# Optimization experiments

Hardware: AMD Instinct MI355X
Metric: run time of the kernel (lower is better)

The kernel has to match this reference:

```python
import jax, jax.numpy as jnp
import numpy as np

N = 32          # objects in the (single) image
P = N * (N - 1) # relation pairs
D = 256         # self.dim
M = 14          # mask_size / pooler resolution
OC = 151        # obj classes
RC = 51         # rel classes
RED = D // 4    # attention gate reduction


def setup_inputs() -> dict:
    key = jax.random.key(0)
    ks = jax.random.split(key, 32)
    # all ordered pairs i != j
    ii, jj = np.meshgrid(np.arange(N), np.arange(N), indexing='ij')
    keep = ii != jj
    rel_pair_idxs = jnp.asarray(np.stack([ii[keep], jj[keep]], 1), jnp.int32)  # [P,2]
    # valid xyxy boxes in an 800x600 image
    x1 = jax.random.uniform(ks[0], (N,)) * 600.0
    y1 = jax.random.uniform(ks[1], (N,)) * 400.0
    w = jax.random.uniform(ks[2], (N,)) * 180.0 + 20.0
    h = jax.random.uniform(ks[3], (N,)) * 180.0 + 20.0
    bboxes = jnp.stack([x1, y1, x1 + w, y1 + h], 1).astype(jnp.float32)
    roi_features = jax.random.normal(ks[4], (N, 4096), jnp.float32)
    predict_logits = jax.random.normal(ks[5], (N, OC), jnp.float32)
    union_features = jax.random.normal(ks[6], (P, D, M, M), jnp.float32)
    s = 0.02
    p = dict(
        roi_features=roi_features, bboxes=bboxes, predict_logits=predict_logits,
        union_features=union_features, rel_pair_idxs=rel_pair_idxs,
        W_emb1=jax.random.normal(ks[7], (4096 + OC + 4, D)) * s, b_emb1=jnp.zeros((D,)),
        W_emb2=jax.random.normal(ks[8], (D, D)) * s, b_emb2=jnp.zeros((D,)),
        # stacked SE-attention gates: 0=sbj, 1=obj, 2=bg
        att_fc1_w=jax.random.normal(ks[9], (3, D, RED)) * s, att_fc1_b=jnp.zeros((3, RED)),
        att_fc2_w=jax.random.normal(ks[10], (3, RED, D)) * s, att_fc2_b=jnp.zeros((3, D)),
        W_c1=jax.random.normal(ks[11], (3 * D, D)) * s, b_c1=jnp.zeros((D,)),
        W_c2=jax.random.normal(ks[12], (D, D)) * s, b_c2=jnp.zeros((D,)),
        W_gcn=jax.random.normal(ks[13], (D, D)) * s, b_gcn=jnp.zeros((D,)),
        W_objp=jax.random.normal(ks[14], (D, OC)) * s, b_objp=jnp.zeros((OC,)),
        W_relp=jax.random.normal(ks[15], (D, RC)) * s, b_relp=jnp.zeros((RC,)),
    )
    return p


def _rect_masks(x0, y0, x1, y1):
    # mask[p, r, c] = 1 iff x0<=r<x1 and y0<=c<y1  (matches torch slice write)
    r = jnp.arange(M, dtype=jnp.float32)
    rm = (r[None, :] >= x0[:, None]) & (r[None, :] < x1[:, None])  # [P,M]
    cm = (r[None, :] >= y0[:, None]) & (r[None, :] < y1[:, None])  # [P,M]
    return (rm[:, :, None] & cm[:, None, :]).astype(jnp.float32)   # [P,M,M]


def _masking(union_features, bboxes, pairs):
    sb = bboxes[pairs[:, 0]]  # [P,4]
    ob = bboxes[pairs[:, 1]]
    ux1 = jnp.minimum(sb[:, 0], ob[:, 0])
    uy1 = jnp.minimum(sb[:, 1], ob[:, 1])
    x = jnp.stack([sb[:, 0], sb[:, 2], ob[:, 0], ob[:, 2]], 1) - ux1[:, None]
    y = jnp.stack([sb[:, 1], sb[:, 3], ob[:, 1], ob[:, 3]], 1) - uy1[:, None]
    xr = M / jnp.maximum(x[:, 1], x[:, 3])
    yr = M / jnp.maximum(y[:, 1], y[:, 3])
    xp = jnp.round(x * xr[:, None])
    yp = jnp.round(y * yr[:, None])
    sm = _rect_masks(xp[:, 0], yp[:, 0], xp[:, 1], yp[:, 1])[:, None]  # [P,1,M,M]
    om = _rect_masks(xp[:, 2], yp[:, 2], xp[:, 3], yp[:, 3])[:, None]
    bm = jnp.clip(1.0 - sm - om, 0.0, 1.0)
    return union_features * sm, union_features * om, union_features * bm


def _att_gate(x, w1, b1, w2, b2):
    # SE-style channel attention gate
    s = x.mean((2, 3))                                        # [P,D]
    g = jax.nn.sigmoid(jax.nn.relu(s @ w1 + b1) @ w2 + b2)    # [P,D]
    return x * g[:, :, None, None]


def _adjacency(pairs):
    o2o = jnp.zeros((N, N)).at[pairs[:, 0], pairs[:, 1]].set(1.0)
    ar = jnp.arange(P)
    o2r = jnp.zeros((N, P)).at[pairs[:, 0], ar].set(1.0).at[pairs[:, 1], ar].set(1.0)
    top = jnp.concatenate([o2o, o2r], 1)                     # [N, N+P]
    bot = jnp.concatenate([o2r.T, jnp.zeros((P, P))], 1)     # [P, N+P]
    adj = jnp.concatenate([top, bot], 0)
    return adj + jnp.eye(N + P)


def reference(roi_features, bboxes, predict_logits, union_features, rel_pair_idxs,
              W_emb1, b_emb1, W_emb2, b_emb2,
              att_fc1_w, att_fc1_b, att_fc2_w, att_fc2_b,
              W_c1, b_c1, W_c2, b_c2, W_gcn, b_gcn,
              W_objp, b_objp, W_relp, b_relp):
    pairs = rel_pair_idxs
    # object embedding
    obj_in = jnp.concatenate([roi_features, predict_logits, bboxes], 1)  # [N,4251]
    obj_feats = jax.nn.relu(obj_in @ W_emb1 + b_emb1) @ W_emb2 + b_emb2  # [N,D]
    # masking + attention gates + global avg pool
    sbj, obj, bg = _masking(union_features, bboxes, pairs)
    sbj = _att_gate(sbj, att_fc1_w[0], att_fc1_b[0], att_fc2_w[0], att_fc2_b[0]).mean((2, 3))
    obj = _att_gate(obj, att_fc1_w[1], att_fc1_b[1], att_fc2_w[1], att_fc2_b[1]).mean((2, 3))
    bg = _att_gate(bg, att_fc1_w[2], att_fc1_b[2], att_fc2_w[2], att_fc2_b[2]).mean((2, 3))
    # relational embedding (compose)
    rel = jnp.concatenate([sbj, obj, bg], 1)                 # [P,3D]
    rel_feats = jax.nn.relu(rel @ W_c1 + b_c1) @ W_c2 + b_c2  # [P,D]
    # GCN over object+relation graph (row-normalized adjacency, residual)
    adj = _adjacency(pairs)
    feats = jnp.concatenate([obj_feats, rel_feats], 0)        # [N+P,D]
    norm_adj = adj / adj.sum(1, keepdims=True)
    gcn_out = jax.nn.relu(norm_adj @ (feats @ W_gcn) + b_gcn) + feats
    obj_dists = gcn_out[:N] @ W_objp + b_objp                 # [N,OC]
    rel_dists = gcn_out[N:] @ W_relp + b_relp                 # [P,RC]
    return obj_dists, rel_dists
```

## Files before the change

### kernel.cpp

```cpp
#include <hip/hip_runtime.h>
#include <cstdint>
#include <cstddef>

#define NOBJ 32
#define NP   992
#define DD   256
#define SP   196
#define OC   151
#define RC   51
#define RED  64
#define KIN  4251
#define CH   128
#define KPC  34

#define OFF_PART   0u
#define OFF_OBJF   1048576u
#define OFF_SALL   1056768u
#define OFF_RELF   1818624u
#define OFF_H      2072576u
#define OFF_W2T    2334720u
#define OFF_WC1T   2400256u
#define OFF_WC2T   2596864u
#define OFF_WGT    2662400u
#define OFF_FC1WT  2727936u
#define OFF_FC2WT  2777088u
#define OFF_WOPT   2826240u
#define OFF_WRPT   2864896u

#define TR_TOT 543232

__global__ void k_pre(const float* __restrict__ uf,
                      const float* __restrict__ bbox,
                      const int* __restrict__ pairs,
                      const float* __restrict__ roi,
                      const float* __restrict__ logits,
                      const float* __restrict__ W1,
                      const float* __restrict__ W2,  const float* __restrict__ Wc1,
                      const float* __restrict__ Wc2, const float* __restrict__ Wg,
                      const float* __restrict__ f1w, const float* __restrict__ f2w,
                      const float* __restrict__ Wop, const float* __restrict__ Wrp,
                      float* __restrict__ sAll, float* __restrict__ part,
                      float* __restrict__ W2T,  float* __restrict__ Wc1T,
                      float* __restrict__ Wc2T, float* __restrict__ WgT,
                      float* __restrict__ f1wT, float* __restrict__ f2wT,
                      float* __restrict__ WopT, float* __restrict__ WrpT) {
  const int b = blockIdx.x, t = threadIdx.x;
  if (b < NP) {
    const int p = b;
    __shared__ __align__(16) float tile[64 * SP + 64];
    __shared__ __align__(16) float wS[256];
    __shared__ __align__(16) float wO[256];
    __shared__ __align__(16) float wB[256];
    __shared__ float pacc[3][4][64];
    if (t < SP) {
      int si = pairs[2 * p], oi = pairs[2 * p + 1];
      float sx1 = bbox[si * 4 + 0], sy1 = bbox[si * 4 + 1];
      float sx2 = bbox[si * 4 + 2], sy2 = bbox[si * 4 + 3];
      float ox1 = bbox[oi * 4 + 0], oy1 = bbox[oi * 4 + 1];
      float ox2 = bbox[oi * 4 + 2], oy2 = bbox[oi * 4 + 3];
      float ux = fminf(sx1, ox1), uy = fminf(sy1, oy1);
      float xr = 14.f / fmaxf(sx2 - ux, ox2 - ux);
      float yr = 14.f / fmaxf(sy2 - uy, oy2 - uy);
      float xs0 = rintf((sx1 - ux) * xr), xs1 = rintf((sx2 - ux) * xr);
      float xo0 = rintf((ox1 - ux) * xr), xo1 = rintf((ox2 - ux) * xr);
      float ys0 = rintf((sy1 - uy) * yr), ys1 = rintf((sy2 - uy) * yr);
      float yo0 = rintf((oy1 - uy) * yr), yo1 = rintf((oy2 - uy) * yr);
      int a = t / 14, bb = t - a * 14;
      float fa = (float)a, fb = (float)bb;
      float sm = (fa >= xs0 && fa < xs1 && fb >= ys0 && fb < ys1) ? 1.f : 0.f;
      float om = (fa >= xo0 && fa < xo1 && fb >= yo0 && fb < yo1) ? 1.f : 0.f;
      float bm = fminf(fmaxf(1.f - sm - om, 0.f), 1.f);
      wS[t] = sm; wO[t] = om; wB[t] = bm;
    } else {
      wS[t] = 0.f; wO[t] = 0.f; wB[t] = 0.f;
    }
    if (t < 64) tile[64 * SP + t] = 0.f;
    __syncthreads();
    const int c = t >> 2, q = t & 3;
    const float* row = tile + c * SP + q * 52;
    const float* mS = wS + q * 52;
    const float* mO = wO + q * 52;
    const float* mB = wB + q * 52;
    const float inv = 1.f / 196.f;
#pragma unroll 1
    for (int ti = 0; ti < 4; ++ti) {
      const float4* src4 = (const float4*)(uf + (size_t)p * (DD * SP) + ti * (64 * SP));
      float4* dst4 = (float4*)tile;
      for (int f = t; f < 64 * SP / 4; f += 256) dst4[f] = src4[f];
      __syncthreads();
      float a0 = 0.f, a1 = 0.f, a2 = 0.f;
#pragma unroll
      for (int g = 0; g < 13; ++g) {
        float4 v  = *(const float4*)&row[4 * g];
        float4 ms = *(const float4*)&mS[4 * g];
        float4 mo = *(const float4*)&mO[4 * g];
        float4 mb = *(const float4*)&mB[4 * g];
        a0 += v.x * ms.x + v.y * ms.y + v.z * ms.z + v.w * ms.w;
        a1 += v.x * mo.x + v.y * mo.y + v.z * mo.z + v.w * mo.w;
        a2 += v.x * mb.x + v.y * mb.y + v.z * mb.z + v.w * mb.w;
      }
      pacc[0][q][c] = a0; pacc[1][q][c] = a1; pacc[2][q][c] = a2;
      __syncthreads();
      if (t < 192) {
        int m = t >> 6, c2 = t & 63;
        float s = pacc[m][0][c2] + pacc[m][1][c2] + pacc[m][2][c2] + pacc[m][3][c2];
        sAll[(size_t)p * 768 + m * 256 + ti * 64 + c2] = s * inv;
      }
      __syncthreads();
    }
  } else if (b < NP + CH) {
    const int chunk = b - NP;
    int k0 = chunk * KPC;
    int k1 = k0 + KPC; if (k1 > KIN) k1 = KIN;
    float acc[NOBJ];
#pragma unroll
    for (int i = 0; i < NOBJ; ++i) acc[i] = 0.f;
#pragma unroll 2
    for (int k = k0; k < k1; ++k) {
      float w = W1[(size_t)k * DD + t];
      const float* xp; int stride;
      if (k < 4096)            { xp = roi    + k;               stride = 4096; }
      else if (k < 4096 + OC)  { xp = logits + (k - 4096);      stride = OC;   }
      else                     { xp = bbox   + (k - 4096 - OC); stride = 4;    }
#pragma unroll
      for (int i = 0; i < NOBJ; ++i) { acc[i] += xp[0] * w; xp += stride; }
    }
    float* pout = part + (size_t)chunk * (NOBJ * DD) + t;
#pragma unroll
    for (int i = 0; i < NOBJ; ++i) pout[i * DD] = acc[i];
  } else {
    for (int o = (b - NP - CH) * 256 + t; o < TR_TOT; o += 256 * 256) {
      float v; float* dst;
      if (o < 65536)       { int q = o;          v = W2 [(q & 255) * 256 + (q >> 8)]; dst = W2T  + q; }
      else if (o < 262144) { int q = o - 65536;  int c = q / 768, k = q - c * 768;
                             v = Wc1[k * 256 + c];                                    dst = Wc1T + q; }
      else if (o < 327680) { int q = o - 262144; v = Wc2[(q & 255) * 256 + (q >> 8)]; dst = Wc2T + q; }
      else if (o < 393216) { int q = o - 327680; v = Wg [(q & 255) * 256 + (q >> 8)]; dst = WgT  + q; }
      else if (o < 442368) { int q = o - 393216;
                             v = f1w[(q >> 14) * 16384 + (q & 255) * 64 + ((q >> 8) & 63)];
                             dst = f1wT + q; }
      else if (o < 491520) { int q = o - 442368;
                             v = f2w[(q >> 14) * 16384 + (q & 63) * 256 + ((q >> 6) & 255)];
                             dst = f2wT + q; }
      else if (o < 530176) { int q = o - 491520; v = Wop[(q & 255) * OC + (q >> 8)];  dst = WopT + q; }
      else                 { int q = o - 530176; v = Wrp[(q & 255) * RC + (q >> 8)];  dst = WrpT + q; }
      *dst = v;
    }
  }
}

__global__ void __launch_bounds__(512, 1)
k_mid2(const float* __restrict__ sAll,
       const float* __restrict__ f1wT, const float* __restrict__ f1b,
       const float* __restrict__ f2wT, const float* __restrict__ f2b,
       const float* __restrict__ Wc1T, const float* __restrict__ bc1,
       const float* __restrict__ Wc2T, const float* __restrict__ bc2,
       const float* __restrict__ WgT,
       const float* __restrict__ part, const float* __restrict__ b1,
       const float* __restrict__ W2T,  const float* __restrict__ b2,
       float* __restrict__ relf, float* __restrict__ objf,
       float* __restrict__ H) {
  const int b = blockIdx.x, t = threadIdx.x;
  const int h = t >> 8, tt = t & 255;
  __shared__ __align__(16) float sg[4][768];
  __shared__ __align__(16) float ha[4][192];
  __shared__ __align__(16) float h2[4][256];
  __shared__ __align__(16) float red[2][4][256];
  if (b < NP / 4) {
    const int p0 = b * 4;
    {
      const float4* src = (const float4*)(sAll + (size_t)p0 * 768);
      float4* dst = (float4*)&sg[0][0];
      for (int j = t; j < 768; j += 512) dst[j] = src[j];
    }
    __syncthreads();
    if (tt < 192) {
      const float4* w4 = (const float4*)(f1wT + tt * 256 + h * 128);
      const int sb = (tt >> 6) * 256 + h * 128;
      float a0 = 0, a1 = 0, a2 = 0, a3 = 0;
#pragma unroll 8
      for (int j = 0; j < 32; ++j) {
        float4 wv = w4[j];
        float4 s0 = *(const float4*)&sg[0][sb + 4 * j];
        float4 s1 = *(const float4*)&sg[1][sb + 4 * j];
        float4 s2 = *(const float4*)&sg[2][sb + 4 * j];
        float4 s3 = *(const float4*)&sg[3][sb + 4 * j];
        a0 += s0.x * wv.x + s0.y * wv.y + s0.z * wv.z + s0.w * wv.w;
        a1 += s1.x * wv.x + s1.y * wv.y + s1.z * wv.z + s1.w * wv.w;
        a2 += s2.x * wv.x + s2.y * wv.y + s2.z * wv.z + s2.w * wv.w;
        a3 += s3.x * wv.x + s3.y * wv.y + s3.z * wv.z + s3.w * wv.w;
      }
      red[h][0][tt] = a0; red[h][1][tt] = a1; red[h][2][tt] = a2; red[h][3][tt] = a3;
    }
    __syncthreads();
    if (h == 0 && tt < 192) {
      float bb = f1b[tt];
#pragma unroll
      for (int p = 0; p < 4; ++p)
        ha[p][tt] = fmaxf(red[0][p][tt] + red[1][p][tt] + bb, 0.f);
    }
    __syncthreads();
    for (int br = 0; br < 3; ++br) {
      const float4* w4 = (const float4*)(f2wT + br * 16384 + tt * 64 + h * 32);
      const int hb = br * 64 + h * 32;
      float a0 = 0, a1 = 0, a2 = 0, a3 = 0;
#pragma unroll
      for (int j = 0; j < 8; ++j) {
        float4 wv = w4[j];
        float4 v0 = *(const float4*)&ha[0][hb + 4 * j];
        float4 v1 = *(const float4*)&ha[1][hb + 4 * j];
        float4 v2 = *(const float4*)&ha[2][hb + 4 * j];
        float4 v3 = *(const float4*)&ha[3][hb + 4 * j];
        a0 += v0.x * wv.x + v0.y * wv.y + v0.z * wv.z + v0.w * wv.w;
        a1 += v1.x * wv.x + v1.y * wv.y + v1.z * wv.z + v1.w * wv.w;
        a2 += v2.x * wv.x + v2.y * wv.y + v2.z * wv.z + v2.w * wv.w;
        a3 += v3.x * wv.x + v3.y * wv.y + v3.z * wv.z + v3.w * wv.w;
      }
      red[h][0][tt] = a0; red[h][1][tt] = a1; red[h][2][tt] = a2; red[h][3][tt] = a3;
      __syncthreads();
      if (h == 0) {
        float bb = f2b[br * 256 + tt];
#pragma unroll
        for (int p = 0; p < 4; ++p) {
          float g = 1.f / (1.f + expf(-(red[0][p][tt] + red[1][p][tt] + bb)));
          sg[p][br * 256 + tt] *= g;
        }
      }
      __syncthreads();
    }
    {
      const float4* w4 = (const float4*)(Wc1T + (size_t)tt * 768 + h * 384);
      const int gb = h * 384;
      float a0 = 0, a1 = 0, a2 = 0, a3 = 0;
#pragma unroll 8
      for (int j = 0; j < 96; ++j) {
        float4 wv = w4[j];
        float4 g0 = *(const float4*)&sg[0][gb + 4 * j];
        float4 g1 = *(const float4*)&sg[1][gb + 4 * j];
        float4 g2 = *(const float4*)&sg[2][gb + 4 * j];
        float4 g3 = *(const float4*)&sg[3][gb + 4 * j];
        a0 += g0.x * wv.x + g0.y * wv.y + g0.z * wv.z + g0.w * wv.w;
        a1 += g1.x * wv.x + g1.y * wv.y + g1.z * wv.z + g1.w * wv.w;
        a2 += g2.x * wv.x + g2.y * wv.y + g2.z * wv.z + g2.w * wv.w;
        a3 += g3.x * wv.x + g3.y * wv.y + g3.z * wv.z + g3.w * wv.w;
      }
      red[h][0][tt] = a0; red[h][1][tt] = a1; red[h][2][tt] = a2; red[h][3][tt] = a3;
    }
    __syncthreads();
    if (h == 0) {
      float bb = bc1[tt];
#pragma unroll
      for (int p = 0; p < 4; ++p)
        h2[p][tt] = fmaxf(red[0][p][tt] + red[1][p][tt] + bb, 0.f);
    }
    __syncthreads();
    {
      const float4* w4 = (const float4*)(Wc2T + (size_t)tt * 256 + h * 128);
      const int hb = h * 128;
      float a0 = 0, a1 = 0, a2 = 0, a3 = 0;
#pragma unroll 8
      for (int j = 0; j < 32; ++j) {
        float4 wv = w4[j];
        float4 v0 = *(const float4*)&h2[0][hb + 4 * j];
        float4 v1 = *(const float4*)&h2[1][hb + 4 * j];
        float4 v2 = *(const float4*)&h2[2][hb + 4 * j];
        float4 v3 = *(const float4*)&h2[3][hb + 4 * j];
        a0 += v0.x * wv.x + v0.y * wv.y + v0.z * wv.z + v0.w * wv.w;
        a1 += v1.x * wv.x + v1.y * wv.y + v1.z * wv.z + v1.w * wv.w;
        a2 += v2.x * wv.x + v2.y * wv.y + v2.z * wv.z + v2.w * wv.w;
        a3 += v3.x * wv.x + v3.y * wv.y + v3.z * wv.z + v3.w * wv.w;
      }
      red[h][0][tt] = a0; red[h][1][tt] = a1; red[h][2][tt] = a2; red[h][3][tt] = a3;
    }
    __syncthreads();
    if (h == 0) {
      float bb = bc2[tt];
#pragma unroll
      for (int p = 0; p < 4; ++p) {
        float v = red[0][p][tt] + red[1][p][tt] + bb;
        relf[(size_t)(p0 + p) * DD + tt] = v;
        sg[p][tt] = v;
      }
    }
    __syncthreads();
    {
      const float4* w4 = (const float4*)(WgT + (size_t)tt * 256 + h * 128);
      const int hb = h * 128;
      float a0 = 0, a1 = 0, a2 = 0, a3 = 0;
#pragma unroll 8
      for (int j = 0; j < 32; ++j) {
        float4 wv = w4[j];
        float4 v0 = *(const float4*)&sg[0][hb + 4 * j];
        float4 v1 = *(const float4*)&sg[1][hb + 4 * j];
        float4 v2 = *(const float4*)&sg[2][hb + 4 * j];
        float4 v3 = *(const float4*)&sg[3][hb + 4 * j];
        a0 += v0.x * wv.x + v0.y * wv.y + v0.z * wv.z + v0.w * wv.w;
        a1 += v1.x * wv.x + v1.y * wv.y + v1.z * wv.z + v1.w * wv.w;
        a2 += v2.x * wv.x + v2.y * wv.y + v2.z * wv.z + v2.w * wv.w;
        a3 += v3.x * wv.x + v3.y * wv.y + v3.z * wv.z + v3.w * wv.w;
      }
      red[h][0][tt] = a0; red[h][1][tt] = a1; red[h][2][tt] = a2; red[h][3][tt] = a3;
    }
    __syncthreads();
    if (h == 0) {
#pragma unroll
      for (int p = 0; p < 4; ++p)
        H[(size_t)(NOBJ + p0 + p) * DD + tt] = red[0][p][tt] + red[1][p][tt];
    }
  } else {
    const int r = (b - NP / 4) * 2 + h;
    float s[8];
#pragma unroll
    for (int u = 0; u < 8; ++u) s[u] = 0.f;
#pragma unroll
    for (int c0 = 0; c0 < CH; c0 += 8) {
#pragma unroll
      for (int u = 0; u < 8; ++u)
        s[u] += part[(size_t)(c0 + u) * (NOBJ * DD) + r * DD + tt];
    }
    float tot = ((s[0] + s[1]) + (s[2] + s[3])) + ((s[4] + s[5]) + (s[6] + s[7]));
    h2[h][tt] = fmaxf(tot + b1[tt], 0.f);
    __syncthreads();
    {
      const float4* w4 = (const float4*)(W2T + (size_t)tt * DD);
      const float* hp = &h2[h][0];
      float a0 = 0, a1 = 0, a2 = 0, a3 = 0;
#pragma unroll 8
      for (int j = 0; j < 64; ++j) {
        float4 wv = w4[j];
        float4 hv = *(const float4*)&hp[4 * j];
        a0 += hv.x * wv.x; a1 += hv.y * wv.y; a2 += hv.z * wv.z; a3 += hv.w * wv.w;
      }
      float v = (a0 + a1) + (a2 + a3) + b2[tt];
      objf[r * DD + tt] = v;
      sg[h][tt] = v;
    }
    __syncthreads();
    {
      const float4* w4 = (const float4*)(WgT + (size_t)tt * DD);
      const float* hp = &sg[h][0];
      float a0 = 0, a1 = 0, a2 = 0, a3 = 0;
#pragma unroll 8
      for (int j = 0; j < 64; ++j) {
        float4 wv = w4[j];
        float4 hv = *(const float4*)&hp[4 * j];
        a0 += hv.x * wv.x; a1 += hv.y * wv.y; a2 += hv.z * wv.z; a3 += hv.w * wv.w;
      }
      H[(size_t)r * DD + tt] = (a0 + a1) + (a2 + a3);
    }
  }
}

__global__ void __launch_bounds__(1024, 1)
k_heads(const float* __restrict__ H, const float* __restrict__ objf,
        const float* __restrict__ relf, const int* __restrict__ pairs,
        const float* __restrict__ bg,
        const float* __restrict__ WopT, const float* __restrict__ bop,
        const float* __restrict__ WrpT, const float* __restrict__ brp,
        float* __restrict__ out) {
  const int b = blockIdx.x, t = threadIdx.x;
  const int p = t >> 8, tt = t & 255;
  if (b < NP / 4) {
    __shared__ __align__(16) float gr[4][DD];
    __shared__ float red[4][4][64];
    const int r = b * 4 + p;
    int si = pairs[2 * r], oi = pairs[2 * r + 1];
    float hsum = H[si * DD + tt] + H[oi * DD + tt] + H[(size_t)(NOBJ + r) * DD + tt];
    gr[p][tt] = fmaxf(hsum * (1.f / 3.f) + bg[tt], 0.f) + relf[(size_t)r * DD + tt];
    __syncthreads();
    const int q = tt >> 6, c = tt & 63;
    float a = 0.f;
    if (c < RC) {
      const float4* w4 = (const float4*)(WrpT + c * 256 + q * 64);
#pragma unroll
      for (int j = 0; j < 16; ++j) {
        float4 wv = w4[j];
        float4 gv = *(const float4*)&gr[p][q * 64 + 4 * j];
        a += gv.x * wv.x + gv.y * wv.y + gv.z * wv.z + gv.w * wv.w;
      }
    }
    red[p][q][c] = a;
    __syncthreads();
    if (tt < RC)
      out[NOBJ * OC + (size_t)r * RC + tt] =
          red[p][0][tt] + red[p][1][tt] + red[p][2][tt] + red[p][3][tt] + brp[tt];
  } else {
    const int i = b - NP / 4;
    const int slice = p;
    __shared__ int2 pr[NP];
    __shared__ float red2[4][DD];
    __shared__ __align__(16) float gro[DD];
    const int2* p2 = (const int2*)pairs;
    for (int r = t; r < NP; r += 1024) pr[r] = p2[r];
    __syncthreads();
    float acc = 0.f;
    if (slice == 0) {
#pragma unroll 8
      for (int j = 0; j < NOBJ; ++j) acc += H[j * DD + tt];
    }
    const int rbeg = slice * 248;
#pragma unroll 8
    for (int r = rbeg; r < rbeg + 248; ++r) {
      int2 q = pr[r];
      float v = H[(size_t)(NOBJ + r) * DD + tt];
      if (q.x == i || q.y == i) acc += v;
    }
    red2[slice][tt] = acc;
    __syncthreads();
    if (t < DD) {
      float pre = (red2[0][t] + red2[1][t] + red2[2][t] + red2[3][t]) * (1.f / 94.f);
      gro[t] = fmaxf(pre + bg[t], 0.f) + objf[i * DD + t];
    }
    __syncthreads();
    float hsum = 0.f;
    if (tt < OC) {
      const float4* w4 = (const float4*)(WopT + tt * 256 + slice * 64);
#pragma unroll
      for (int j = 0; j < 16; ++j) {
        float4 wv = w4[j];
        float4 gv = *(const float4*)&gro[slice * 64 + 4 * j];
        hsum += gv.x * wv.x + gv.y * wv.y + gv.z * wv.z + gv.w * wv.w;
      }
    }
    red2[slice][tt] = hsum;
    __syncthreads();
    if (t < OC)
      out[i * OC + t] = red2[0][t] + red2[1][t] + red2[2][t] + red2[3][t] + bop[t];
  }
}

extern "C" void kernel_launch(void* const* d_in, const int* in_sizes, int n_in,
                              void* d_out, int out_size, void* d_ws, size_t ws_size,
                              hipStream_t stream) {
  const float* roi   = (const float*)d_in[0];
  const float* bbox  = (const float*)d_in[1];
  const float* logit = (const float*)d_in[2];
  const float* uf    = (const float*)d_in[3];
  const int*   pairs = (const int*)d_in[4];
  const float* W1    = (const float*)d_in[5];
  const float* b1    = (const float*)d_in[6];
  const float* W2    = (const float*)d_in[7];
  const float* b2    = (const float*)d_in[8];
  const float* fc1w  = (const float*)d_in[9];
  const float* fc1b  = (const float*)d_in[10];
  const float* fc2w  = (const float*)d_in[11];
  const float* fc2b  = (const float*)d_in[12];
  const float* Wc1   = (const float*)d_in[13];
  const float* bc1   = (const float*)d_in[14];
  const float* Wc2   = (const float*)d_in[15];
  const float* bc2   = (const float*)d_in[16];
  const float* Wg    = (const float*)d_in[17];
  const float* bg    = (const float*)d_in[18];
  const float* Wop   = (const float*)d_in[19];
  const float* bop   = (const float*)d_in[20];
  const float* Wrp   = (const float*)d_in[21];
  const float* brp   = (const float*)d_in[22];

  float* ws    = (float*)d_ws;
  float* part  = ws + OFF_PART;
  float* objf  = ws + OFF_OBJF;
  float* sAll  = ws + OFF_SALL;
  float* relf  = ws + OFF_RELF;
  float* Hbuf  = ws + OFF_H;
  float* W2T   = ws + OFF_W2T;
  float* Wc1T  = ws + OFF_WC1T;
  float* Wc2T  = ws + OFF_WC2T;
  float* WgT   = ws + OFF_WGT;
  float* f1wT  = ws + OFF_FC1WT;
  float* f2wT  = ws + OFF_FC2WT;
  float* WopT  = ws + OFF_WOPT;
  float* WrpT  = ws + OFF_WRPT;
  float* out   = (float*)d_out;

  k_pre<<<NP + CH + 256, 256, 0, stream>>>(uf, bbox, pairs, roi, logit, W1,
                                           W2, Wc1, Wc2, Wg, fc1w, fc2w, Wop, Wrp,
                                           sAll, part, W2T, Wc1T, Wc2T, WgT,
                                           f1wT, f2wT, WopT, WrpT);
  k_mid2<<<NP / 4 + 16, 512, 0, stream>>>(sAll, f1wT, fc1b, f2wT, fc2b,
                                          Wc1T, bc1, Wc2T, bc2, WgT,
                                          part, b1, W2T, b2, relf, objf, Hbuf);
  k_heads<<<NP / 4 + NOBJ, 1024, 0, stream>>>(Hbuf, objf, relf, pairs, bg,
                                              WopT, bop, WrpT, brp, out);
}
```

Measured before the change: 525.7 us.

## Shrink pooling tile to 32 channels and prefetch next tile into registers

The masked-pooling stage now stages 32 channels at a time (about 25 KB of LDS instead of about 50 KB), so more blocks fit per CU, and it sets launch bounds for 5 blocks per CU. The next tile's global loads are issued into registers before the current tile is computed, overlapping HBM latency with the compute. The cross-thread reduction moves from an LDS partial array plus extra barriers to wavefront shuffles over 8 lanes. The costs are more registers per thread for the prefetch buffer and twice as many tile iterations.

```diff
diff --git a/kernel.cpp b/kernel.cpp
--- a/kernel.cpp
+++ b/kernel.cpp
@@ -29,84 +29,107 @@
 
 #define TR_TOT 543232
 
-__global__ void k_pre(const float* __restrict__ uf,
-                      const float* __restrict__ bbox,
-                      const int* __restrict__ pairs,
-                      const float* __restrict__ roi,
-                      const float* __restrict__ logits,
-                      const float* __restrict__ W1,
-                      const float* __restrict__ W2,  const float* __restrict__ Wc1,
-                      const float* __restrict__ Wc2, const float* __restrict__ Wg,
-                      const float* __restrict__ f1w, const float* __restrict__ f2w,
-                      const float* __restrict__ Wop, const float* __restrict__ Wrp,
-                      float* __restrict__ sAll, float* __restrict__ part,
-                      float* __restrict__ W2T,  float* __restrict__ Wc1T,
-                      float* __restrict__ Wc2T, float* __restrict__ WgT,
-                      float* __restrict__ f1wT, float* __restrict__ f2wT,
-                      float* __restrict__ WopT, float* __restrict__ WrpT) {
+#define TCH  32
+#define NTIL 8
+#define TF4  1568
+
+__global__ void __launch_bounds__(256, 5)
+k_pre(const float* __restrict__ uf,
+      const float* __restrict__ bbox,
+      const int* __restrict__ pairs,
+      const float* __restrict__ roi,
+      const float* __restrict__ logits,
+      const float* __restrict__ W1,
+      const float* __restrict__ W2,  const float* __restrict__ Wc1,
+      const float* __restrict__ Wc2, const float* __restrict__ Wg,
+      const float* __restrict__ f1w, const float* __restrict__ f2w,
+      const float* __restrict__ Wop, const float* __restrict__ Wrp,
+      float* __restrict__ sAll, float* __restrict__ part,
+      float* __restrict__ W2T,  float* __restrict__ Wc1T,
+      float* __restrict__ Wc2T, float* __restrict__ WgT,
+      float* __restrict__ f1wT, float* __restrict__ f2wT,
+      float* __restrict__ WopT, float* __restrict__ WrpT) {
   const int b = blockIdx.x, t = threadIdx.x;
   if (b < NP) {
     const int p = b;
-    __shared__ __align__(16) float tile[64 * SP + 64];
-    __shared__ __align__(16) float wS[256];
-    __shared__ __align__(16) float wO[256];
-    __shared__ __align__(16) float wB[256];
-    __shared__ float pacc[3][4][64];
-    if (t < SP) {
-      int si = pairs[2 * p], oi = pairs[2 * p + 1];
-      float sx1 = bbox[si * 4 + 0], sy1 = bbox[si * 4 + 1];
-      float sx2 = bbox[si * 4 + 2], sy2 = bbox[si * 4 + 3];
-      float ox1 = bbox[oi * 4 + 0], oy1 = bbox[oi * 4 + 1];
-      float ox2 = bbox[oi * 4 + 2], oy2 = bbox[oi * 4 + 3];
-      float ux = fminf(sx1, ox1), uy = fminf(sy1, oy1);
-      float xr = 14.f / fmaxf(sx2 - ux, ox2 - ux);
-      float yr = 14.f / fmaxf(sy2 - uy, oy2 - uy);
-      float xs0 = rintf((sx1 - ux) * xr), xs1 = rintf((sx2 - ux) * xr);
-      float xo0 = rintf((ox1 - ux) * xr), xo1 = rintf((ox2 - ux) * xr);
-      float ys0 = rintf((sy1 - uy) * yr), ys1 = rintf((sy2 - uy) * yr);
-      float yo0 = rintf((oy1 - uy) * yr), yo1 = rintf((oy2 - uy) * yr);
-      int a = t / 14, bb = t - a * 14;
-      float fa = (float)a, fb = (float)bb;
-      float sm = (fa >= xs0 && fa < xs1 && fb >= ys0 && fb < ys1) ? 1.f : 0.f;
-      float om = (fa >= xo0 && fa < xo1 && fb >= yo0 && fb < yo1) ? 1.f : 0.f;
-      float bm = fminf(fmaxf(1.f - sm - om, 0.f), 1.f);
-      wS[t] = sm; wO[t] = om; wB[t] = bm;
-    } else {
-      wS[t] = 0.f; wO[t] = 0.f; wB[t] = 0.f;
-    }
-    if (t < 64) tile[64 * SP + t] = 0.f;
-    __syncthreads();
-    const int c = t >> 2, q = t & 3;
-    const float* row = tile + c * SP + q * 52;
-    const float* mS = wS + q * 52;
-    const float* mO = wO + q * 52;
-    const float* mB = wB + q * 52;
+    __shared__ __align__(16) float buf[TCH * SP + 28];
+    __shared__ __align__(16) float mS[224];
+    __shared__ __align__(16) float mO[224];
+    __shared__ __align__(16) float mB[224];
+    if (t < 224) {
+      float sm = 0.f, om = 0.f, bm = 0.f;
+      if (t < SP) {
+        int si = pairs[2 * p], oi = pairs[2 * p + 1];
+        float sx1 = bbox[si * 4 + 0], sy1 = bbox[si * 4 + 1];
+        float sx2 = bbox[si * 4 + 2], sy2 = bbox[si * 4 + 3];
+        float ox1 = bbox[oi * 4 + 0], oy1 = bbox[oi * 4 + 1];
+        float ox2 = bbox[oi * 4 + 2], oy2 = bbox[oi * 4 + 3];
+        float ux = fminf(sx1, ox1), uy = fminf(sy1, oy1);
+        float xr = 14.f / fmaxf(sx2 - ux, ox2 - ux);
+        float yr = 14.f / fmaxf(sy2 - uy, oy2 - uy);
+        float xs0 = rintf((sx1 - ux) * xr), xs1 = rintf((sx2 - ux) * xr);
+        float xo0 = rintf((ox1 - ux) * xr), xo1 = rintf((ox2 - ux) * xr);
+        float ys0 = rintf((sy1 - uy) * yr), ys1 = rintf((sy2 - uy) * yr);
+        float yo0 = rintf((oy1 - uy) * yr), yo1 = rintf((oy2 - uy) * yr);
+        int a = t / 14, bb = t - a * 14;
+        float fa = (float)a, fb = (float)bb;
+        sm = (fa >= xs0 && fa < xs1 && fb >= ys0 && fb < ys1) ? 1.f : 0.f;
+        om = (fa >= xo0 && fa < xo1 && fb >= yo0 && fb < yo1) ? 1.f : 0.f;
+        bm = fminf(fmaxf(1.f - sm - om, 0.f), 1.f);
+      }
+      mS[t] = sm; mO[t] = om; mB[t] = bm;
+    }
+    if (t < 28) buf[TCH * SP + t] = 0.f;
+    const float4* base4 = (const float4*)(uf + (size_t)p * (DD * SP));
+    {
+      const float4* src = base4 + t;
+      float4* dst = (float4*)buf + t;
+      dst[0] = src[0];     dst[256] = src[256];   dst[512] = src[512];
+      dst[768] = src[768]; dst[1024] = src[1024]; dst[1280] = src[1280];
+      if (t < 32) dst[1536] = src[1536];
+    }
+    __syncthreads();
+    const int cl = t >> 3, o = t & 7;
+    const float* row = buf + cl * SP + o * 28;
+    const float* msp = mS + o * 28;
+    const float* mop = mO + o * 28;
+    const float* mbp = mB + o * 28;
     const float inv = 1.f / 196.f;
+    float4 s0, s1, s2, s3, s4, s5, s6 = {0.f, 0.f, 0.f, 0.f};
 #pragma unroll 1
-    for (int ti = 0; ti < 4; ++ti) {
-      const float4* src4 = (const float4*)(uf + (size_t)p * (DD * SP) + ti * (64 * SP));
-      float4* dst4 = (float4*)tile;
-      for (int f = t; f < 64 * SP / 4; f += 256) dst4[f] = src4[f];
-      __syncthreads();
-      float a0 = 0.f, a1 = 0.f, a2 = 0.f;
-#pragma unroll
-      for (int g = 0; g < 13; ++g) {
-        float4 v  = *(const float4*)&row[4 * g];
-        float4 ms = *(const float4*)&mS[4 * g];
-        float4 mo = *(const float4*)&mO[4 * g];
-        float4 mb = *(const float4*)&mB[4 * g];
-        a0 += v.x * ms.x + v.y * ms.y + v.z * ms.z + v.w * ms.w;
-        a1 += v.x * mo.x + v.y * mo.y + v.z * mo.z + v.w * mo.w;
-        a2 += v.x * mb.x + v.y * mb.y + v.z * mb.z + v.w * mb.w;
-      }
-      pacc[0][q][c] = a0; pacc[1][q][c] = a1; pacc[2][q][c] = a2;
-      __syncthreads();
-      if (t < 192) {
-        int m = t >> 6, c2 = t & 63;
-        float s = pacc[m][0][c2] + pacc[m][1][c2] + pacc[m][2][c2] + pacc[m][3][c2];
-        sAll[(size_t)p * 768 + m * 256 + ti * 64 + c2] = s * inv;
-      }
-      __syncthreads();
+    for (int ti = 0; ti < NTIL; ++ti) {
+      if (ti < NTIL - 1) {
+        const float4* src = base4 + (ti + 1) * TF4 + t;
+        s0 = src[0];     s1 = src[256];   s2 = src[512];
+        s3 = src[768];   s4 = src[1024];  s5 = src[1280];
+        if (t < 32) s6 = src[1536];
+      }
+      float aS = 0.f, aO = 0.f, aB = 0.f;
+#pragma unroll
+      for (int j = 0; j < 7; ++j) {
+        float4 v = *(const float4*)&row[4 * j];
+        float4 x = *(const float4*)&msp[4 * j];
+        float4 y = *(const float4*)&mop[4 * j];
+        float4 z = *(const float4*)&mbp[4 * j];
+        aS += v.x * x.x + v.y * x.y + v.z * x.z + v.w * x.w;
+        aO += v.x * y.x + v.y * y.y + v.z * y.z + v.w * y.w;
+        aB += v.x * z.x + v.y * z.y + v.z * z.z + v.w * z.w;
+      }
+      aS += __shfl_xor(aS, 1); aS += __shfl_xor(aS, 2); aS += __shfl_xor(aS, 4);
+      aO += __shfl_xor(aO, 1); aO += __shfl_xor(aO, 2); aO += __shfl_xor(aO, 4);
+      aB += __shfl_xor(aB, 1); aB += __shfl_xor(aB, 2); aB += __shfl_xor(aB, 4);
+      const int ch = ti * TCH + cl;
+      if (o == 0)      sAll[(size_t)p * 768 + ch]       = aS * inv;
+      else if (o == 1) sAll[(size_t)p * 768 + 256 + ch] = aO * inv;
+      else if (o == 2) sAll[(size_t)p * 768 + 512 + ch] = aB * inv;
+      if (ti < NTIL - 1) {
+        __syncthreads();
+        float4* dst = (float4*)buf + t;
+        dst[0] = s0;     dst[256] = s1;   dst[512] = s2;
+        dst[768] = s3;   dst[1024] = s4;  dst[1280] = s5;
+        if (t < 32) dst[1536] = s6;
+        __syncthreads();
+      }
     }
   } else if (b < NP + CH) {
     const int chunk = b - NP;
```

Result: faster. 498.6 us (-5.2%).
